# Performance work log

Measured on AMD Instinct MI355X. Metric: run time of the kernel, lower is better.

## Reference

```python
import jax, jax.numpy as jnp
import numpy as np

B, S, D = 4, 4096, 1024
E, I = 8, 2048
CAPACITY = 2
K = max(1, int(S / E * CAPACITY))  # tokens per expert per batch element


def setup_inputs() -> dict:
    key = jax.random.key(0)
    k1, k2, k3, k4, k5 = jax.random.split(key, 5)
    x = jax.random.normal(k1, (B, S, D), dtype=jnp.float32)
    gate_w = jax.random.normal(k2, (D, E), dtype=jnp.float32) * 0.006
    Wg = jax.random.normal(k3, (E, D, I), dtype=jnp.float32) * 0.02
    Wu = jax.random.normal(k4, (E, D, I), dtype=jnp.float32) * 0.02
    Wd = jax.random.normal(k5, (E, I, D), dtype=jnp.float32) * 0.02
    return {"x": x, "gate_w": gate_w, "Wg": Wg, "Wu": Wu, "Wd": Wd}


def reference(x, gate_w, Wg, Wu, Wd):
    # Router: softmax over experts per token, then per-expert top-k tokens.
    logits = jnp.einsum('bsd,de->bse', x, gate_w)          # [B,S,E]
    affinity = jax.nn.softmax(logits, axis=-1)
    affinity_T = jnp.transpose(affinity, (0, 2, 1))        # [B,E,S]
    gating, index = jax.lax.top_k(affinity_T, K)           # [B,E,K]

    # Gather selected tokens for all experts at once: [B,E,K,D]
    b_idx = jnp.arange(x.shape[0])[:, None, None]
    x_sel = x[b_idx, index]

    # Per-expert SwiGLU MLP (grouped GEMMs over the expert axis).
    g = jnp.einsum('bekd,edi->beki', x_sel, Wg)
    u = jnp.einsum('bekd,edi->beki', x_sel, Wu)
    h = jax.nn.silu(g) * u
    out = jnp.einsum('beki,eid->bekd', h, Wd)              # [B,E,K,D]

    # Weighted scatter-add combine back to token positions.
    contrib = out * gating[..., None]
    x_out = jnp.zeros_like(x).at[b_idx, index].add(contrib)
    return x_out
```

## Files before the change

kernel.cpp:

```cpp
#include <hip/hip_runtime.h>

#define B_ 4
#define S_ 4096
#define D_ 1024
#define E_ 8
#define I_ 2048
#define K_ 1024

typedef __attribute__((ext_vector_type(8))) short short8;
typedef __attribute__((ext_vector_type(4))) float f32x4;

__device__ __forceinline__ short f2bf(float f) {
  union { float f; unsigned u; } v; v.f = f;
  unsigned r = v.u + 0x7FFFu + ((v.u >> 16) & 1u);
  return (short)(r >> 16);
}

__device__ __forceinline__ void gload16(const void* g, void* l) {
  __builtin_amdgcn_global_load_lds((const __attribute__((address_space(1))) unsigned int*)g,
                                   (__attribute__((address_space(3))) unsigned int*)l, 16, 0, 0);
}

__device__ __forceinline__ short8 rdswz(const short* ls, int row, int cb) {
  int byte = (row << 7) + (cb ^ ((row & 7) << 4));
  return *reinterpret_cast<const short8*>(reinterpret_cast<const char*>(ls) + byte);
}

__global__ __launch_bounds__(256) void router_kernel(const float* __restrict__ x,
                                                     const float* __restrict__ gw,
                                                     double* __restrict__ affD) {
  int wave = threadIdx.x >> 6, lane = threadIdx.x & 63;
  int tok = blockIdx.x * 4 + wave;
  int b = tok >> 12, s = tok & (S_ - 1);
  const float* xr = x + (size_t)tok * D_;
  double acc[E_];
#pragma unroll
  for (int e = 0; e < E_; ++e) acc[e] = 0.0;
#pragma unroll 4
  for (int r = 0; r < 16; ++r) {
    int d = r * 64 + lane;
    float xv = xr[d];
    const float4* g4 = reinterpret_cast<const float4*>(gw + (size_t)d * E_);
    float4 g0 = g4[0], g1 = g4[1];
    acc[0] += (double)xv * g0.x; acc[1] += (double)xv * g0.y;
    acc[2] += (double)xv * g0.z; acc[3] += (double)xv * g0.w;
    acc[4] += (double)xv * g1.x; acc[5] += (double)xv * g1.y;
    acc[6] += (double)xv * g1.z; acc[7] += (double)xv * g1.w;
  }
#pragma unroll
  for (int off = 32; off > 0; off >>= 1) {
#pragma unroll
    for (int e = 0; e < E_; ++e) acc[e] += __shfl_xor(acc[e], off, 64);
  }
  double m = acc[0];
#pragma unroll
  for (int e = 1; e < E_; ++e) m = acc[e] > m ? acc[e] : m;
  double den = 0.0, ex[E_];
#pragma unroll
  for (int e = 0; e < E_; ++e) { ex[e] = exp(acc[e] - m); den += ex[e]; }
  if (lane < E_)
    affD[((size_t)b * E_ + lane) * S_ + s] = ex[lane] / den;
}

__global__ __launch_bounds__(1024) void topk_select_kernel(const double* __restrict__ affD,
                                                           int* __restrict__ idxArr,
                                                           float* __restrict__ gateArr) {
  __shared__ unsigned hist[256];
  __shared__ unsigned s_digit;
  __shared__ int s_rem;
  __shared__ unsigned s_cnt;
  int be = blockIdx.x, tid = threadIdx.x;
  const double* a = affD + (size_t)be * S_;
  unsigned long long key[4];
  bool active[4];
#pragma unroll
  for (int c = 0; c < 4; ++c) {
    int i = tid + c * 1024;
    unsigned long long kb = (unsigned long long)__double_as_longlong(a[i]);
    key[c] = (kb & ~0xFFFULL) | (unsigned long long)(4095 - i);
    active[c] = true;
  }
  int remk = K_;
  unsigned long long prefix = 0;
  for (int pass = 0; pass < 8; ++pass) {
    int shift = 56 - pass * 8;
    if (tid < 256) hist[tid] = 0;
    __syncthreads();
#pragma unroll
    for (int c = 0; c < 4; ++c)
      if (active[c]) atomicAdd(&hist[(unsigned)((key[c] >> shift) & 0xFF)], 1u);
    __syncthreads();
    if (tid == 0) {
      unsigned cum = 0; int d = 255;
      for (; d > 0; --d) {
        unsigned h = hist[d];
        if (cum + h >= (unsigned)remk) break;
        cum += h;
      }
      s_digit = (unsigned)d;
      s_rem = remk - (int)cum;
    }
    __syncthreads();
    unsigned dg = s_digit; remk = s_rem;
    prefix |= ((unsigned long long)dg) << shift;
#pragma unroll
    for (int c = 0; c < 4; ++c)
      active[c] = active[c] && (((key[c] >> shift) & 0xFF) == dg);
    __syncthreads();
  }
  if (tid == 0) s_cnt = 0;
  __syncthreads();
#pragma unroll
  for (int c = 0; c < 4; ++c) {
    if (key[c] >= prefix) {
      unsigned slot = atomicAdd(&s_cnt, 1u);
      int i = 4095 - (int)(key[c] & 0xFFF);
      idxArr[(size_t)be * K_ + slot] = i;
      gateArr[(size_t)be * K_ + slot] = (float)a[i];
    }
  }
}

__global__ __launch_bounds__(256) void transpose_cvt_kernel(const float* __restrict__ in,
                                                            unsigned short* __restrict__ out,
                                                            int M, int N) {
  __shared__ float t[64][65];
  int e = blockIdx.y;
  int ntn = N >> 6;
  int tm = (blockIdx.x / ntn) << 6;
  int tn = (blockIdx.x % ntn) << 6;
  const float* src = in + (size_t)e * M * N;
  unsigned short* dst = out + (size_t)e * M * N;
  int tid = threadIdx.x;
#pragma unroll
  for (int it = 0; it < 4; ++it) {
    int f = it * 256 + tid;
    int r = f >> 4, c4 = (f & 15) << 2;
    float4 v = *reinterpret_cast<const float4*>(&src[(size_t)(tm + r) * N + tn + c4]);
    t[c4][r] = v.x; t[c4 + 1][r] = v.y; t[c4 + 2][r] = v.z; t[c4 + 3][r] = v.w;
  }
  __syncthreads();
#pragma unroll
  for (int it = 0; it < 4; ++it) {
    int f = it * 256 + tid;
    int rr = f >> 4, c4 = (f & 15) << 2;
    short4 o;
    o.x = f2bf(t[rr][c4]); o.y = f2bf(t[rr][c4 + 1]);
    o.z = f2bf(t[rr][c4 + 2]); o.w = f2bf(t[rr][c4 + 3]);
    *reinterpret_cast<short4*>(&dst[(size_t)(tn + rr) * M + tm + c4]) = o;
  }
}

__global__ __launch_bounds__(256) void gather_cvt_kernel(const float* __restrict__ x,
                                                         const int* __restrict__ idxArr,
                                                         unsigned short* __restrict__ Xsel) {
  int row = blockIdx.x * 4 + (threadIdx.x >> 6);
  int lane = threadIdx.x & 63;
  int b = row >> 13;
  int tok = idxArr[row];
  const float* src = x + ((size_t)b * S_ + tok) * D_;
  unsigned short* dst = Xsel + (size_t)row * D_;
#pragma unroll
  for (int it = 0; it < 4; ++it) {
    int d = it * 256 + lane * 4;
    float4 v = *reinterpret_cast<const float4*>(src + d);
    short4 o;
    o.x = f2bf(v.x); o.y = f2bf(v.y); o.z = f2bf(v.z); o.w = f2bf(v.w);
    *reinterpret_cast<short4*>(dst + d) = o;
  }
}

__global__ __launch_bounds__(512, 2) void mlp1_kernel(
    const unsigned short* __restrict__ Xsel, const unsigned short* __restrict__ WgT,
    const unsigned short* __restrict__ WuT, unsigned short* __restrict__ H,
    int Ic, int i0) {
  const int Nt = Ic >> 7;
  int nwg = gridDim.x;
  int bid = (blockIdx.x & 7) * (nwg >> 3) + (blockIdx.x >> 3);
  int nt = bid % Nt; bid /= Nt;
  int mt = bid & 3; bid >>= 2;
  int be = bid;
  int e = be & 7;

  __shared__ short lsA[2][256 * 64];
  __shared__ short lsB[2][256 * 64];

  int tid = threadIdx.x, w = tid >> 6, lane = tid & 63;
  int wm = w >> 2, wn = w & 3;
  int lr = lane & 15, lg = lane >> 4;
  int srow = lane >> 3;
  int scol = ((lane & 7) ^ srow) << 4;

  const char* pa = (const char*)(Xsel + ((size_t)be * K_ + mt * 256) * D_);
  const char* pg = (const char*)(WgT + ((size_t)e * I_ + i0 + nt * 128) * D_);
  const char* pu = (const char*)(WuT + ((size_t)e * I_ + i0 + nt * 128) * D_);

  auto STAGE = [&](int t) {
    int buf = t & 1;
    int kb = t * 128;
#pragma unroll
    for (int ch = 0; ch < 4; ++ch) {
      int rb = ch * 64 + w * 8;
      int r = rb + srow;
      gload16(pa + (size_t)r * 2048 + kb + scol, (char*)(&lsA[buf][0]) + rb * 128);
      int hu = (r >> 4) & 1;
      int iloc = ((r >> 5) << 4) + (r & 15);
      const char* pb = hu ? pu : pg;
      gload16(pb + (size_t)iloc * 2048 + kb + scol, (char*)(&lsB[buf][0]) + rb * 128);
    }
  };

  f32x4 acc[8][4];
#pragma unroll
  for (int i = 0; i < 8; ++i)
#pragma unroll
    for (int j = 0; j < 4; ++j) acc[i][j] = (f32x4){0.f, 0.f, 0.f, 0.f};

  const int NT = 16;
  STAGE(0);
  STAGE(1);
  asm volatile("s_waitcnt vmcnt(8) lgkmcnt(0)" ::: "memory");
  __builtin_amdgcn_s_barrier();

  for (int t = 0; t < NT; ++t) {
    const short* A = &lsA[t & 1][0];
    const short* Bt = &lsB[t & 1][0];
    short8 af0[8], bf0[4];
#pragma unroll
    for (int fm = 0; fm < 8; ++fm) af0[fm] = rdswz(A, wm * 128 + fm * 16 + lr, lg * 16);
#pragma unroll
    for (int fn = 0; fn < 4; ++fn) bf0[fn] = rdswz(Bt, wn * 64 + fn * 16 + lr, lg * 16);
    __builtin_amdgcn_s_setprio(1);
#pragma unroll
    for (int fm = 0; fm < 8; ++fm)
#pragma unroll
      for (int fn = 0; fn < 4; ++fn)
        acc[fm][fn] = __builtin_amdgcn_mfma_f32_16x16x32_bf16(af0[fm], bf0[fn], acc[fm][fn], 0, 0, 0);
    __builtin_amdgcn_s_setprio(0);
    short8 af1[8], bf1[4];
#pragma unroll
    for (int fm = 0; fm < 8; ++fm) af1[fm] = rdswz(A, wm * 128 + fm * 16 + lr, 64 + lg * 16);
#pragma unroll
    for (int fn = 0; fn < 4; ++fn) bf1[fn] = rdswz(Bt, wn * 64 + fn * 16 + lr, 64 + lg * 16);
    asm volatile("s_waitcnt lgkmcnt(0)" ::: "memory");
    __builtin_amdgcn_s_barrier();
    if (t + 2 < NT) STAGE(t + 2);
    __builtin_amdgcn_s_setprio(1);
#pragma unroll
    for (int fm = 0; fm < 8; ++fm)
#pragma unroll
      for (int fn = 0; fn < 4; ++fn)
        acc[fm][fn] = __builtin_amdgcn_mfma_f32_16x16x32_bf16(af1[fm], bf1[fn], acc[fm][fn], 0, 0, 0);
    __builtin_amdgcn_s_setprio(0);
    if (t + 1 < NT) {
      if (t + 2 < NT) asm volatile("s_waitcnt vmcnt(8)" ::: "memory");
      else            asm volatile("s_waitcnt vmcnt(0)" ::: "memory");
      __builtin_amdgcn_s_barrier();
    }
  }

  unsigned short* Hbe = H + (size_t)be * K_ * Ic;
#pragma unroll
  for (int fm = 0; fm < 8; ++fm)
#pragma unroll
    for (int q = 0; q < 2; ++q)
#pragma unroll
      for (int j = 0; j < 4; ++j) {
        float g = acc[fm][2 * q][j], u = acc[fm][2 * q + 1][j];
        float h = g / (1.f + __expf(-g)) * u;
        int row = mt * 256 + wm * 128 + fm * 16 + lg * 4 + j;
        int col = nt * 128 + (wn * 2 + q) * 16 + lr;
        Hbe[(size_t)row * Ic + col] = (unsigned short)f2bf(h);
      }
}

__global__ __launch_bounds__(512, 2) void mlp2_kernel(
    const unsigned short* __restrict__ H, const unsigned short* __restrict__ WdT,
    const int* __restrict__ idxArr, const float* __restrict__ gateArr,
    float* __restrict__ out, int Ic, int i0) {
  int nwg = gridDim.x;
  int bid = (blockIdx.x & 7) * (nwg >> 3) + (blockIdx.x >> 3);
  int nt = bid & 3; bid >>= 2;
  int mt = bid & 3; bid >>= 2;
  int be = bid;
  int b = be >> 3, e = be & 7;

  __shared__ short lsA[2][256 * 64];
  __shared__ short lsB[2][256 * 64];
  __shared__ int sTok[256];
  __shared__ float sGate[256];

  int tid = threadIdx.x, w = tid >> 6, lane = tid & 63;
  int wm = w >> 2, wn = w & 3;
  int lr = lane & 15, lg = lane >> 4;
  int srow = lane >> 3;
  int scol = ((lane & 7) ^ srow) << 4;

  if (tid < 256) {
    size_t gbase = (size_t)be * K_ + mt * 256 + tid;
    sTok[tid] = idxArr[gbase];
    sGate[tid] = gateArr[gbase];
  }

  const char* pa = (const char*)(H + ((size_t)be * K_ + mt * 256) * Ic);
  const char* pb = (const char*)(WdT + ((size_t)e * D_ + nt * 256) * I_ + i0);
  size_t strideA = (size_t)Ic * 2;

  auto STAGE = [&](int t) {
    int buf = t & 1;
    int kb = t * 128;
#pragma unroll
    for (int ch = 0; ch < 4; ++ch) {
      int rb = ch * 64 + w * 8;
      int r = rb + srow;
      gload16(pa + (size_t)r * strideA + kb + scol, (char*)(&lsA[buf][0]) + rb * 128);
      gload16(pb + (size_t)r * 4096 + kb + scol, (char*)(&lsB[buf][0]) + rb * 128);
    }
  };

  f32x4 acc[8][4];
#pragma unroll
  for (int i = 0; i < 8; ++i)
#pragma unroll
    for (int j = 0; j < 4; ++j) acc[i][j] = (f32x4){0.f, 0.f, 0.f, 0.f};

  const int NT = Ic >> 6;
  STAGE(0);
  STAGE(1);
  asm volatile("s_waitcnt vmcnt(8) lgkmcnt(0)" ::: "memory");
  __builtin_amdgcn_s_barrier();

  for (int t = 0; t < NT; ++t) {
    const short* A = &lsA[t & 1][0];
    const short* Bt = &lsB[t & 1][0];
    short8 af0[8], bf0[4];
#pragma unroll
    for (int fm = 0; fm < 8; ++fm) af0[fm] = rdswz(A, wm * 128 + fm * 16 + lr, lg * 16);
#pragma unroll
    for (int fn = 0; fn < 4; ++fn) bf0[fn] = rdswz(Bt, wn * 64 + fn * 16 + lr, lg * 16);
    __builtin_amdgcn_s_setprio(1);
#pragma unroll
    for (int fm = 0; fm < 8; ++fm)
#pragma unroll
      for (int fn = 0; fn < 4; ++fn)
        acc[fm][fn] = __builtin_amdgcn_mfma_f32_16x16x32_bf16(af0[fm], bf0[fn], acc[fm][fn], 0, 0, 0);
    __builtin_amdgcn_s_setprio(0);
    short8 af1[8], bf1[4];
#pragma unroll
    for (int fm = 0; fm < 8; ++fm) af1[fm] = rdswz(A, wm * 128 + fm * 16 + lr, 64 + lg * 16);
#pragma unroll
    for (int fn = 0; fn < 4; ++fn) bf1[fn] = rdswz(Bt, wn * 64 + fn * 16 + lr, 64 + lg * 16);
    asm volatile("s_waitcnt lgkmcnt(0)" ::: "memory");
    __builtin_amdgcn_s_barrier();
    if (t + 2 < NT) STAGE(t + 2);
    __builtin_amdgcn_s_setprio(1);
#pragma unroll
    for (int fm = 0; fm < 8; ++fm)
#pragma unroll
      for (int fn = 0; fn < 4; ++fn)
        acc[fm][fn] = __builtin_amdgcn_mfma_f32_16x16x32_bf16(af1[fm], bf1[fn], acc[fm][fn], 0, 0, 0);
    __builtin_amdgcn_s_setprio(0);
    if (t + 1 < NT) {
      if (t + 2 < NT) asm volatile("s_waitcnt vmcnt(8)" ::: "memory");
      else            asm volatile("s_waitcnt vmcnt(0)" ::: "memory");
      __builtin_amdgcn_s_barrier();
    }
  }

#pragma unroll
  for (int fm = 0; fm < 8; ++fm)
#pragma unroll
    for (int fn = 0; fn < 4; ++fn) {
#pragma unroll
      for (int j = 0; j < 4; ++j) {
        int row = wm * 128 + fm * 16 + lg * 4 + j;
        int col = nt * 256 + wn * 64 + fn * 16 + lr;
        float v = acc[fm][fn][j] * sGate[row];
        atomicAdd(&out[((size_t)b * S_ + sTok[row]) * D_ + col], v);
      }
    }
}

extern "C" void kernel_launch(void* const* d_in, const int* in_sizes, int n_in,
                              void* d_out, int out_size, void* d_ws, size_t ws_size,
                              hipStream_t stream) {
  const float* x  = (const float*)d_in[0];
  const float* gw = (const float*)d_in[1];
  const float* Wg = (const float*)d_in[2];
  const float* Wu = (const float*)d_in[3];
  const float* Wd = (const float*)d_in[4];
  float* out = (float*)d_out;
  char* ws = (char*)d_ws;

  size_t off = 0;
  double* affD = (double*)(ws + off); off += (size_t)B_ * E_ * S_ * sizeof(double);
  int* idxArr = (int*)(ws + off);     off += (size_t)B_ * E_ * K_ * sizeof(int);
  float* gateArr = (float*)(ws + off); off += (size_t)B_ * E_ * K_ * sizeof(float);
  off = (off + 255) & ~(size_t)255;
  unsigned short* WgT = (unsigned short*)(ws + off); off += (size_t)E_ * D_ * I_ * 2;
  unsigned short* WuT = (unsigned short*)(ws + off); off += (size_t)E_ * D_ * I_ * 2;
  unsigned short* WdT = (unsigned short*)(ws + off); off += (size_t)E_ * D_ * I_ * 2;
  unsigned short* Xsel = (unsigned short*)(ws + off); off += (size_t)B_ * E_ * K_ * D_ * 2;
  off = (off + 255) & ~(size_t)255;
  unsigned short* H = (unsigned short*)(ws + off);
  size_t rem = (ws_size > off) ? (ws_size - off) : 0;

  int Ic = 128;
  for (int c = I_; c >= 128; c >>= 1) {
    if ((size_t)B_ * E_ * K_ * (size_t)c * 2 <= rem) { Ic = c; break; }
  }

  hipMemsetAsync(d_out, 0, (size_t)out_size * sizeof(float), stream);
  router_kernel<<<B_ * S_ / 4, 256, 0, stream>>>(x, gw, affD);
  topk_select_kernel<<<B_ * E_, 1024, 0, stream>>>(affD, idxArr, gateArr);
  transpose_cvt_kernel<<<dim3((D_ / 64) * (I_ / 64), E_), 256, 0, stream>>>(Wg, WgT, D_, I_);
  transpose_cvt_kernel<<<dim3((D_ / 64) * (I_ / 64), E_), 256, 0, stream>>>(Wu, WuT, D_, I_);
  transpose_cvt_kernel<<<dim3((I_ / 64) * (D_ / 64), E_), 256, 0, stream>>>(Wd, WdT, I_, D_);
  gather_cvt_kernel<<<B_ * E_ * K_ / 4, 256, 0, stream>>>(x, idxArr, Xsel);
  for (int i0 = 0; i0 < I_; i0 += Ic) {
    mlp1_kernel<<<B_ * E_ * 4 * (Ic / 128), 512, 0, stream>>>(Xsel, WgT, WuT, H, Ic, i0);
    mlp2_kernel<<<B_ * E_ * 4 * 4, 512, 0, stream>>>(H, WdT, idxArr, gateArr, out, Ic, i0);
  }
}
```

Baseline: 834.2 us.

## Split GEMM main loop into four quadrant phases with interleaved half-tile prefetch

Both MLP GEMM kernels now run each K-tile as four quadrant sub-phases (rows 0-3/4-7 by cols 0-1/2-3), each issuing a quarter-tile global-to-LDS prefetch between barriers. LDS staging is split into row halves matched to the quadrant order, so the B second half of tile t+1 and the A/B halves of tile t+2 are loaded while MFMAs run. This fine-grained ping-pong aims to smooth memory issue and shrink register pressure from holding full fragment sets. The cost is more barriers per iteration and tricky vmcnt accounting, which risks stalls or races.

```diff
diff --git a/kernel.cpp b/kernel.cpp
--- a/kernel.cpp
+++ b/kernel.cpp
@@ -9,6 +9,9 @@
 
 typedef __attribute__((ext_vector_type(8))) short short8;
 typedef __attribute__((ext_vector_type(4))) float f32x4;
+
+#define PH_BAR() asm volatile("s_barrier" ::: "memory")
+#define LGKM0()  asm volatile("s_waitcnt lgkmcnt(0)" ::: "memory")
 
 __device__ __forceinline__ short f2bf(float f) {
   union { float f; unsigned u; } v; v.f = f;
@@ -184,29 +187,40 @@
 
   __shared__ short lsA[2][256 * 64];
   __shared__ short lsB[2][256 * 64];
+  char* lsAb = (char*)&lsA[0][0];
+  char* lsBb = (char*)&lsB[0][0];
 
   int tid = threadIdx.x, w = tid >> 6, lane = tid & 63;
   int wm = w >> 2, wn = w & 3;
   int lr = lane & 15, lg = lane >> 4;
-  int srow = lane >> 3;
-  int scol = ((lane & 7) ^ srow) << 4;
 
   const char* pa = (const char*)(Xsel + ((size_t)be * K_ + mt * 256) * D_);
   const char* pg = (const char*)(WgT + ((size_t)e * I_ + i0 + nt * 128) * D_);
   const char* pu = (const char*)(WuT + ((size_t)e * I_ + i0 + nt * 128) * D_);
 
-  auto STAGE = [&](int t) {
-    int buf = t & 1;
-    int kb = t * 128;
-#pragma unroll
-    for (int ch = 0; ch < 4; ++ch) {
-      int rb = ch * 64 + w * 8;
-      int r = rb + srow;
-      gload16(pa + (size_t)r * 2048 + kb + scol, (char*)(&lsA[buf][0]) + rb * 128);
+  auto STAGE_A = [&](int t, int half) {
+    int buf = t & 1, kb = t * 128;
+#pragma unroll
+    for (int s = 0; s < 2; ++s) {
+      int rl0 = s * 64 + w * 8;
+      int r0 = (half ? 64 : 0) + ((rl0 & 63) + ((rl0 >> 6) << 7));
+      int r = r0 + (lane >> 3);
+      int sc = ((lane & 7) ^ (r & 7)) << 4;
+      gload16(pa + (size_t)r * 2048 + kb + sc, lsAb + buf * 32768 + r0 * 128);
+    }
+  };
+  auto STAGE_B = [&](int t, int half) {
+    int buf = t & 1, kb = t * 128;
+#pragma unroll
+    for (int s = 0; s < 2; ++s) {
+      int rl0 = s * 64 + w * 8;
+      int r0 = (half ? 32 : 0) + ((rl0 >> 5) << 6) + (rl0 & 31);
+      int r = r0 + (lane >> 3);
       int hu = (r >> 4) & 1;
       int iloc = ((r >> 5) << 4) + (r & 15);
-      const char* pb = hu ? pu : pg;
-      gload16(pb + (size_t)iloc * 2048 + kb + scol, (char*)(&lsB[buf][0]) + rb * 128);
+      int sc = ((lane & 7) ^ (r & 7)) << 4;
+      const char* srcb = hu ? pu : pg;
+      gload16(srcb + (size_t)iloc * 2048 + kb + sc, lsBb + buf * 32768 + r0 * 128);
     }
   };
 
@@ -217,46 +231,88 @@
     for (int j = 0; j < 4; ++j) acc[i][j] = (f32x4){0.f, 0.f, 0.f, 0.f};
 
   const int NT = 16;
-  STAGE(0);
-  STAGE(1);
-  asm volatile("s_waitcnt vmcnt(8) lgkmcnt(0)" ::: "memory");
-  __builtin_amdgcn_s_barrier();
-
+  __syncthreads();
+  STAGE_A(0, 0); STAGE_B(0, 0); STAGE_A(0, 1); STAGE_B(0, 1);
+  STAGE_A(1, 0); STAGE_B(1, 0); STAGE_A(1, 1);
+  asm volatile("s_waitcnt vmcnt(6)" ::: "memory");
+  PH_BAR();
+
+#pragma unroll 1
   for (int t = 0; t < NT; ++t) {
     const short* A = &lsA[t & 1][0];
     const short* Bt = &lsB[t & 1][0];
-    short8 af0[8], bf0[4];
-#pragma unroll
-    for (int fm = 0; fm < 8; ++fm) af0[fm] = rdswz(A, wm * 128 + fm * 16 + lr, lg * 16);
-#pragma unroll
-    for (int fn = 0; fn < 4; ++fn) bf0[fn] = rdswz(Bt, wn * 64 + fn * 16 + lr, lg * 16);
-    __builtin_amdgcn_s_setprio(1);
-#pragma unroll
-    for (int fm = 0; fm < 8; ++fm)
-#pragma unroll
-      for (int fn = 0; fn < 4; ++fn)
-        acc[fm][fn] = __builtin_amdgcn_mfma_f32_16x16x32_bf16(af0[fm], bf0[fn], acc[fm][fn], 0, 0, 0);
-    __builtin_amdgcn_s_setprio(0);
-    short8 af1[8], bf1[4];
-#pragma unroll
-    for (int fm = 0; fm < 8; ++fm) af1[fm] = rdswz(A, wm * 128 + fm * 16 + lr, 64 + lg * 16);
-#pragma unroll
-    for (int fn = 0; fn < 4; ++fn) bf1[fn] = rdswz(Bt, wn * 64 + fn * 16 + lr, 64 + lg * 16);
-    asm volatile("s_waitcnt lgkmcnt(0)" ::: "memory");
-    __builtin_amdgcn_s_barrier();
-    if (t + 2 < NT) STAGE(t + 2);
-    __builtin_amdgcn_s_setprio(1);
-#pragma unroll
-    for (int fm = 0; fm < 8; ++fm)
-#pragma unroll
-      for (int fn = 0; fn < 4; ++fn)
-        acc[fm][fn] = __builtin_amdgcn_mfma_f32_16x16x32_bf16(af1[fm], bf1[fn], acc[fm][fn], 0, 0, 0);
+    short8 a03[4][2], a47[4][2], b[2][2];
+#pragma unroll
+    for (int fm = 0; fm < 4; ++fm) {
+      a03[fm][0] = rdswz(A, wm * 128 + fm * 16 + lr, lg * 16);
+      a03[fm][1] = rdswz(A, wm * 128 + fm * 16 + lr, 64 + lg * 16);
+    }
+#pragma unroll
+    for (int fn = 0; fn < 2; ++fn) {
+      b[fn][0] = rdswz(Bt, wn * 64 + fn * 16 + lr, lg * 16);
+      b[fn][1] = rdswz(Bt, wn * 64 + fn * 16 + lr, 64 + lg * 16);
+    }
+    if (t + 1 < NT) STAGE_B(t + 1, 1);
+    PH_BAR(); LGKM0();
+    __builtin_amdgcn_s_setprio(1);
+#pragma unroll
+    for (int fm = 0; fm < 4; ++fm)
+#pragma unroll
+      for (int fn = 0; fn < 2; ++fn) {
+        acc[fm][fn] = __builtin_amdgcn_mfma_f32_16x16x32_bf16(a03[fm][0], b[fn][0], acc[fm][fn], 0, 0, 0);
+        acc[fm][fn] = __builtin_amdgcn_mfma_f32_16x16x32_bf16(a03[fm][1], b[fn][1], acc[fm][fn], 0, 0, 0);
+      }
+    __builtin_amdgcn_s_setprio(0);
+    PH_BAR();
+#pragma unroll
+    for (int fm = 0; fm < 4; ++fm) {
+      a47[fm][0] = rdswz(A, wm * 128 + (4 + fm) * 16 + lr, lg * 16);
+      a47[fm][1] = rdswz(A, wm * 128 + (4 + fm) * 16 + lr, 64 + lg * 16);
+    }
+    if (t + 2 < NT) STAGE_A(t + 2, 0);
+    PH_BAR(); LGKM0();
+    __builtin_amdgcn_s_setprio(1);
+#pragma unroll
+    for (int fm = 0; fm < 4; ++fm)
+#pragma unroll
+      for (int fn = 0; fn < 2; ++fn) {
+        acc[4 + fm][fn] = __builtin_amdgcn_mfma_f32_16x16x32_bf16(a47[fm][0], b[fn][0], acc[4 + fm][fn], 0, 0, 0);
+        acc[4 + fm][fn] = __builtin_amdgcn_mfma_f32_16x16x32_bf16(a47[fm][1], b[fn][1], acc[4 + fm][fn], 0, 0, 0);
+      }
+    __builtin_amdgcn_s_setprio(0);
+    PH_BAR();
+#pragma unroll
+    for (int fn = 0; fn < 2; ++fn) {
+      b[fn][0] = rdswz(Bt, wn * 64 + (2 + fn) * 16 + lr, lg * 16);
+      b[fn][1] = rdswz(Bt, wn * 64 + (2 + fn) * 16 + lr, 64 + lg * 16);
+    }
+    if (t + 2 < NT) STAGE_B(t + 2, 0);
+    PH_BAR(); LGKM0();
+    __builtin_amdgcn_s_setprio(1);
+#pragma unroll
+    for (int fm = 0; fm < 4; ++fm)
+#pragma unroll
+      for (int fn = 0; fn < 2; ++fn) {
+        acc[4 + fm][2 + fn] = __builtin_amdgcn_mfma_f32_16x16x32_bf16(a47[fm][0], b[fn][0], acc[4 + fm][2 + fn], 0, 0, 0);
+        acc[4 + fm][2 + fn] = __builtin_amdgcn_mfma_f32_16x16x32_bf16(a47[fm][1], b[fn][1], acc[4 + fm][2 + fn], 0, 0, 0);
+      }
+    __builtin_amdgcn_s_setprio(0);
+    PH_BAR();
+    if (t + 2 < NT) STAGE_A(t + 2, 1);
+    __builtin_amdgcn_s_setprio(1);
+#pragma unroll
+    for (int fm = 0; fm < 4; ++fm)
+#pragma unroll
+      for (int fn = 0; fn < 2; ++fn) {
+        acc[fm][2 + fn] = __builtin_amdgcn_mfma_f32_16x16x32_bf16(a03[fm][0], b[fn][0], acc[fm][2 + fn], 0, 0, 0);
+        acc[fm][2 + fn] = __builtin_amdgcn_mfma_f32_16x16x32_bf16(a03[fm][1], b[fn][1], acc[fm][2 + fn], 0, 0, 0);
+      }
     __builtin_amdgcn_s_setprio(0);
     if (t + 1 < NT) {
-      if (t + 2 < NT) asm volatile("s_waitcnt vmcnt(8)" ::: "memory");
+      if (t + 2 < NT) asm volatile("s_waitcnt vmcnt(6)" ::: "memory");
       else            asm volatile("s_waitcnt vmcnt(0)" ::: "memory");
-      __builtin_amdgcn_s_barrier();
-    }
+    }
+    PH_BAR();
   }
 
   unsigned short* Hbe = H + (size_t)be * K_ * Ic;
@@ -289,12 +345,12 @@
   __shared__ short lsB[2][256 * 64];
   __shared__ int sTok[256];
   __shared__ float sGate[256];
+  char* lsAb = (char*)&lsA[0][0];
+  char* lsBb = (char*)&lsB[0][0];
 
   int tid = threadIdx.x, w = tid >> 6, lane = tid & 63;
   int wm = w >> 2, wn = w & 3;
   int lr = lane & 15, lg = lane >> 4;
-  int srow = lane >> 3;
-  int scol = ((lane & 7) ^ srow) << 4;
 
   if (tid < 256) {
     size_t gbase = (size_t)be * K_ + mt * 256 + tid;
@@ -304,19 +360,30 @@
 
   const char* pa = (const char*)(H + ((size_t)be * K_ + mt * 256) * Ic);
   const char* pb = (const char*)(WdT + ((size_t)e * D_ + nt * 256) * I_ + i0);
-  size_t strideA = (size_t)Ic * 2;
-
-  auto STAGE = [&](int t) {
-    int buf = t & 1;
-    int kb = t * 128;
-#pragma unroll
-    for (int ch = 0; ch < 4; ++ch) {
-      int rb = ch * 64 + w * 8;
-      int r = rb + srow;
-      gload16(pa + (size_t)r * strideA + kb + scol, (char*)(&lsA[buf][0]) + rb * 128);
-      gload16(pb + (size_t)r * 4096 + kb + scol, (char*)(&lsB[buf][0]) + rb * 128);
+  size_t sA = (size_t)Ic * 2;
+
+  auto STAGE_A = [&](int t, int half) {
+    int buf = t & 1, kb = t * 128;
+#pragma unroll
+    for (int s = 0; s < 2; ++s) {
+      int rl0 = s * 64 + w * 8;
+      int r0 = (half ? 64 : 0) + ((rl0 & 63) + ((rl0 >> 6) << 7));
+      int r = r0 + (lane >> 3);
+      int sc = ((lane & 7) ^ (r & 7)) << 4;
+      gload16(pa + (size_t)r * sA + kb + sc, lsAb + buf * 32768 + r0 * 128);
     }
   };
+  auto STAGE_B = [&](int t, int half) {
+    int buf = t & 1, kb = t * 128;
+#pragma unroll
+    for (int s = 0; s < 2; ++s) {
+      int rl0 = s * 64 + w * 8;
+      int r0 = (half ? 32 : 0) + ((rl0 >> 5) << 6) + (rl0 & 31);
+      int r = r0 + (lane >> 3);
+      int sc = ((lane & 7) ^ (r & 7)) << 4;
+      gload16(pb + (size_t)r * 4096 + kb + sc, lsBb + buf * 32768 + r0 * 128);
+    }
+  };
 
   f32x4 acc[8][4];
 #pragma unroll
@@ -325,46 +392,88 @@
     for (int j = 0; j < 4; ++j) acc[i][j] = (f32x4){0.f, 0.f, 0.f, 0.f};
 
   const int NT = Ic >> 6;
-  STAGE(0);
-  STAGE(1);
-  asm volatile("s_waitcnt vmcnt(8) lgkmcnt(0)" ::: "memory");
-  __builtin_amdgcn_s_barrier();
-
+  __syncthreads();
+  STAGE_A(0, 0); STAGE_B(0, 0); STAGE_A(0, 1); STAGE_B(0, 1);
+  STAGE_A(1, 0); STAGE_B(1, 0); STAGE_A(1, 1);
+  asm volatile("s_waitcnt vmcnt(6)" ::: "memory");
+  PH_BAR();
+
+#pragma unroll 1
   for (int t = 0; t < NT; ++t) {
     const short* A = &lsA[t & 1][0];
     const short* Bt = &lsB[t & 1][0];
-    short8 af0[8], bf0[4];
-#pragma unroll
-    for (int fm = 0; fm < 8; ++fm) af0[fm] = rdswz(A, wm * 128 + fm * 16 + lr, lg * 16);
-#pragma unroll
-    for (int fn = 0; fn < 4; ++fn) bf0[fn] = rdswz(Bt, wn * 64 + fn * 16 + lr, lg * 16);
-    __builtin_amdgcn_s_setprio(1);
-#pragma unroll
-    for (int fm = 0; fm < 8; ++fm)
-#pragma unroll
-      for (int fn = 0; fn < 4; ++fn)
-        acc[fm][fn] = __builtin_amdgcn_mfma_f32_16x16x32_bf16(af0[fm], bf0[fn], acc[fm][fn], 0, 0, 0);
-    __builtin_amdgcn_s_setprio(0);
-    short8 af1[8], bf1[4];
-#pragma unroll
-    for (int fm = 0; fm < 8; ++fm) af1[fm] = rdswz(A, wm * 128 + fm * 16 + lr, 64 + lg * 16);
-#pragma unroll
-    for (int fn = 0; fn < 4; ++fn) bf1[fn] = rdswz(Bt, wn * 64 + fn * 16 + lr, 64 + lg * 16);
-    asm volatile("s_waitcnt lgkmcnt(0)" ::: "memory");
-    __builtin_amdgcn_s_barrier();
-    if (t + 2 < NT) STAGE(t + 2);
-    __builtin_amdgcn_s_setprio(1);
-#pragma unroll
-    for (int fm = 0; fm < 8; ++fm)
-#pragma unroll
-      for (int fn = 0; fn < 4; ++fn)
-        acc[fm][fn] = __builtin_amdgcn_mfma_f32_16x16x32_bf16(af1[fm], bf1[fn], acc[fm][fn], 0, 0, 0);
+    short8 a03[4][2], a47[4][2], b[2][2];
+#pragma unroll
+    for (int fm = 0; fm < 4; ++fm) {
+      a03[fm][0] = rdswz(A, wm * 128 + fm * 16 + lr, lg * 16);
+      a03[fm][1] = rdswz(A, wm * 128 + fm * 16 + lr, 64 + lg * 16);
+    }
+#pragma unroll
+    for (int fn = 0; fn < 2; ++fn) {
+      b[fn][0] = rdswz(Bt, wn * 64 + fn * 16 + lr, lg * 16);
+      b[fn][1] = rdswz(Bt, wn * 64 + fn * 16 + lr, 64 + lg * 16);
+    }
+    if (t + 1 < NT) STAGE_B(t + 1, 1);
+    PH_BAR(); LGKM0();
+    __builtin_amdgcn_s_setprio(1);
+#pragma unroll
+    for (int fm = 0; fm < 4; ++fm)
+#pragma unroll
+      for (int fn = 0; fn < 2; ++fn) {
+        acc[fm][fn] = __builtin_amdgcn_mfma_f32_16x16x32_bf16(a03[fm][0], b[fn][0], acc[fm][fn], 0, 0, 0);
+        acc[fm][fn] = __builtin_amdgcn_mfma_f32_16x16x32_bf16(a03[fm][1], b[fn][1], acc[fm][fn], 0, 0, 0);
+      }
+    __builtin_amdgcn_s_setprio(0);
+    PH_BAR();
+#pragma unroll
+    for (int fm = 0; fm < 4; ++fm) {
+      a47[fm][0] = rdswz(A, wm * 128 + (4 + fm) * 16 + lr, lg * 16);
+      a47[fm][1] = rdswz(A, wm * 128 + (4 + fm) * 16 + lr, 64 + lg * 16);
+    }
+    if (t + 2 < NT) STAGE_A(t + 2, 0);
+    PH_BAR(); LGKM0();
+    __builtin_amdgcn_s_setprio(1);
+#pragma unroll
+    for (int fm = 0; fm < 4; ++fm)
+#pragma unroll
+      for (int fn = 0; fn < 2; ++fn) {
+        acc[4 + fm][fn] = __builtin_amdgcn_mfma_f32_16x16x32_bf16(a47[fm][0], b[fn][0], acc[4 + fm][fn], 0, 0, 0);
+        acc[4 + fm][fn] = __builtin_amdgcn_mfma_f32_16x16x32_bf16(a47[fm][1], b[fn][1], acc[4 + fm][fn], 0, 0, 0);
+      }
+    __builtin_amdgcn_s_setprio(0);
+    PH_BAR();
+#pragma unroll
+    for (int fn = 0; fn < 2; ++fn) {
+      b[fn][0] = rdswz(Bt, wn * 64 + (2 + fn) * 16 + lr, lg * 16);
+      b[fn][1] = rdswz(Bt, wn * 64 + (2 + fn) * 16 + lr, 64 + lg * 16);
+    }
+    if (t + 2 < NT) STAGE_B(t + 2, 0);
+    PH_BAR(); LGKM0();
+    __builtin_amdgcn_s_setprio(1);
+#pragma unroll
+    for (int fm = 0; fm < 4; ++fm)
+#pragma unroll
+      for (int fn = 0; fn < 2; ++fn) {
+        acc[4 + fm][2 + fn] = __builtin_amdgcn_mfma_f32_16x16x32_bf16(a47[fm][0], b[fn][0], acc[4 + fm][2 + fn], 0, 0, 0);
+        acc[4 + fm][2 + fn] = __builtin_amdgcn_mfma_f32_16x16x32_bf16(a47[fm][1], b[fn][1], acc[4 + fm][2 + fn], 0, 0, 0);
+      }
+    __builtin_amdgcn_s_setprio(0);
+    PH_BAR();
+    if (t + 2 < NT) STAGE_A(t + 2, 1);
+    __builtin_amdgcn_s_setprio(1);
+#pragma unroll
+    for (int fm = 0; fm < 4; ++fm)
+#pragma unroll
+      for (int fn = 0; fn < 2; ++fn) {
+        acc[fm][2 + fn] = __builtin_amdgcn_mfma_f32_16x16x32_bf16(a03[fm][0], b[fn][0], acc[fm][2 + fn], 0, 0, 0);
+        acc[fm][2 + fn] = __builtin_amdgcn_mfma_f32_16x16x32_bf16(a03[fm][1], b[fn][1], acc[fm][2 + fn], 0, 0, 0);
+      }
     __builtin_amdgcn_s_setprio(0);
     if (t + 1 < NT) {
-      if (t + 2 < NT) asm volatile("s_waitcnt vmcnt(8)" ::: "memory");
+      if (t + 2 < NT) asm volatile("s_waitcnt vmcnt(6)" ::: "memory");
       else            asm volatile("s_waitcnt vmcnt(0)" ::: "memory");
-      __builtin_amdgcn_s_barrier();
-    }
+    }
+    PH_BAR();
   }
 
 #pragma unroll
```

After: 826.8 us. Within noise of the previous version (-0.9%).
